# Kernel tuning notes

Measured on AMD Instinct MI355X. Metric: run time of the kernel, lower is better.

## Reference

```python
import jax, jax.numpy as jnp
import numpy as np

HIDDEN = 1024
STATE = 16
EXPAND = 2
INNER = HIDDEN * EXPAND
BATCH, SEQ = 4, 2048


def setup_inputs() -> dict:
    key = jax.random.key(0)
    ks = jax.random.split(key, 12)
    s = 0.02
    return {
        "x": jax.random.normal(ks[0], (BATCH, SEQ, HIDDEN), jnp.float32),
        "norm_scale": jnp.ones((HIDDEN,), jnp.float32),
        "norm_bias": jnp.zeros((HIDDEN,), jnp.float32),
        "W_in": jax.random.normal(ks[1], (HIDDEN, 2 * INNER), jnp.float32) * s,
        "conv_w": jax.random.normal(ks[2], (INNER, 3), jnp.float32) * 0.3,
        "conv_b": jnp.zeros((INNER,), jnp.float32),
        "W_dt": jax.random.normal(ks[3], (INNER, INNER), jnp.float32) * s,
        "b_dt": jnp.zeros((INNER,), jnp.float32),
        "A_log": jax.random.normal(ks[4], (INNER, STATE), jnp.float32),
        "D_param": jnp.ones((INNER,), jnp.float32),
        "W_B": jax.random.normal(ks[5], (INNER, STATE), jnp.float32) * s,
        "W_C": jax.random.normal(ks[6], (INNER, STATE), jnp.float32) * s,
        "W_out": jax.random.normal(ks[7], (INNER, HIDDEN), jnp.float32) * s,
    }


def reference(x, norm_scale, norm_bias, W_in, conv_w, conv_b, W_dt, b_dt,
              A_log, D_param, W_B, W_C, W_out):
    residual = x
    # LayerNorm (eps = 1e-5, matches nn.LayerNorm default)
    mu = jnp.mean(x, axis=-1, keepdims=True)
    var = jnp.mean(jnp.square(x - mu), axis=-1, keepdims=True)
    xn = (x - mu) * jax.lax.rsqrt(var + 1e-5) * norm_scale + norm_bias

    xz = xn @ W_in                         # [B, L, 2*inner]
    xb, z = jnp.split(xz, 2, axis=-1)      # each [B, L, inner]

    # depthwise conv1d, kernel 3, padding 1 (cross-correlation as in torch)
    xp = jnp.pad(xb, ((0, 0), (1, 1), (0, 0)))
    xb = (conv_w[:, 0] * xp[:, :-2] + conv_w[:, 1] * xp[:, 1:-1]
          + conv_w[:, 2] * xp[:, 2:] + conv_b)
    xb = jax.nn.silu(xb)

    dt = jax.nn.softplus(xb @ W_dt + b_dt)  # [B, L, inner]
    A = -jnp.exp(A_log)                     # [inner, N]
    Bi = xb @ W_B                           # [B, L, N]
    Ci = xb @ W_C                           # [B, L, N]

    def step(h, inp):
        x_t, dt_t, B_t, C_t = inp           # [B,D], [B,D], [B,N], [B,N]
        A_bar = jnp.exp(dt_t[:, :, None] * A)                 # [B, D, N]
        h = A_bar * h + (dt_t * x_t)[:, :, None] * B_t[:, None, :]
        y_t = jnp.einsum('bdn,bn->bd', h, C_t)
        return h, y_t

    h0 = jnp.zeros((x.shape[0], INNER, STATE), x.dtype)
    xs = (jnp.swapaxes(xb, 0, 1), jnp.swapaxes(dt, 0, 1),
          jnp.swapaxes(Bi, 0, 1), jnp.swapaxes(Ci, 0, 1))
    _, y = jax.lax.scan(step, h0, xs)       # y: [L, B, D]
    y = jnp.swapaxes(y, 0, 1)

    y = (y + D_param * xb) * jax.nn.silu(z)
    return residual + y @ W_out
```

## Files before the change

### kernel.cpp

```cpp
#include <hip/hip_runtime.h>
#include <hip/hip_bf16.h>
#include <cstdint>
#include <cstddef>

#define B_DIM 4
#define L_DIM 2048
#define H_DIM 1024
#define D_DIM 2048
#define N_STATE 16
#define TOKENS (B_DIM * L_DIM)
#define CH 16
#define LC (L_DIM / CH)
#define NEXT 2304
#define NLIM2 2080

typedef __bf16 bf16x8 __attribute__((ext_vector_type(8)));
typedef float f32x4 __attribute__((ext_vector_type(4)));

__device__ __forceinline__ float sigmoidf_(float x) { return 1.f / (1.f + __expf(-x)); }
__device__ __forceinline__ float softplusf_(float x) {
  return fmaxf(x, 0.f) + log1pf(__expf(-fabsf(x)));
}
__device__ __forceinline__ void gl_lds16(const void* g, void* l) {
  __builtin_amdgcn_global_load_lds(
      (const __attribute__((address_space(1))) unsigned int*)g,
      (__attribute__((address_space(3))) unsigned int*)l, 16, 0, 0);
}

__global__ __launch_bounds__(256) void ln_kernel(const float* __restrict__ x,
    const float* __restrict__ gamma, const float* __restrict__ beta,
    __hip_bfloat16* __restrict__ out) {
  int row = blockIdx.x;
  int t = threadIdx.x;
  const float* px = x + (size_t)row * H_DIM;
  float4 v = *(const float4*)(px + t * 4);
  float s  = v.x + v.y + v.z + v.w;
  float ss = v.x * v.x + v.y * v.y + v.z * v.z + v.w * v.w;
  for (int off = 32; off > 0; off >>= 1) {
    s  += __shfl_down(s, off);
    ss += __shfl_down(ss, off);
  }
  __shared__ float red[8];
  __shared__ float stats[2];
  int wave = t >> 6, lane = t & 63;
  if (lane == 0) { red[wave] = s; red[4 + wave] = ss; }
  __syncthreads();
  if (t == 0) {
    float S  = red[0] + red[1] + red[2] + red[3];
    float SS = red[4] + red[5] + red[6] + red[7];
    float mu = S / H_DIM;
    float var = SS / H_DIM - mu * mu;
    stats[0] = mu;
    stats[1] = rsqrtf(var + 1e-5f);
  }
  __syncthreads();
  float mu = stats[0], rstd = stats[1];
  float4 g  = *(const float4*)(gamma + t * 4);
  float4 bt = *(const float4*)(beta + t * 4);
  __hip_bfloat16* po = out + (size_t)row * H_DIM + t * 4;
  po[0] = __float2bfloat16((v.x - mu) * rstd * g.x + bt.x);
  po[1] = __float2bfloat16((v.y - mu) * rstd * g.y + bt.y);
  po[2] = __float2bfloat16((v.z - mu) * rstd * g.z + bt.z);
  po[3] = __float2bfloat16((v.w - mu) * rstd * g.w + bt.w);
}

__global__ void transpose_bf16(const float* __restrict__ in,
                               __hip_bfloat16* __restrict__ out, int R, int C) {
  __shared__ float tile[32][33];
  int c0 = blockIdx.x * 32, r0 = blockIdx.y * 32;
  int tx = threadIdx.x, ty = threadIdx.y;
  for (int i = 0; i < 32; i += 8)
    tile[ty + i][tx] = in[(size_t)(r0 + ty + i) * C + c0 + tx];
  __syncthreads();
  for (int i = 0; i < 32; i += 8)
    out[(size_t)(c0 + ty + i) * R + r0 + tx] = __float2bfloat16(tile[tx][ty + i]);
}

__global__ __launch_bounds__(256) void wbc_transpose(const float* __restrict__ WB,
    const float* __restrict__ WC, __hip_bfloat16* __restrict__ Wext) {
  int tid = blockIdx.x * 256 + threadIdx.x;
  int c = tid & 31;
  int k0 = (tid >> 5) * 16;
  const float* W = (c < 16) ? WB : WC;
  int cc = c & 15;
  __hip_bfloat16* o = Wext + (size_t)(2048 + c) * D_DIM + k0;
  for (int kk = 0; kk < 16; ++kk)
    o[kk] = __float2bfloat16(W[(size_t)(k0 + kk) * N_STATE + cc]);
}

template <int MODE>
__global__ __launch_bounds__(512, 2) void gemm256(
    const __hip_bfloat16* __restrict__ A, const __hip_bfloat16* __restrict__ Bt,
    void* __restrict__ C0, void* __restrict__ C1, int nsplit, int nlimit,
    int K, int lda, int ldb, int ldc, int ntn,
    const float* __restrict__ bias, const float* __restrict__ resid) {
  __shared__ __hip_bfloat16 lds[65536];
  const int t = threadIdx.x;
  const int nwg = gridDim.x;
  int bid = blockIdx.x;
  int wgid = (bid & 7) * (nwg >> 3) + (bid >> 3);
  const int m0 = (wgid / ntn) * 256;
  const int n0 = (wgid % ntn) * 256;

  const int wave = t >> 6, lane = t & 63;
  const int wm = wave >> 2, wn = wave & 3;
  const int l16 = lane & 15, quad = lane >> 4;
  const int bh = wn >> 1;

  const int srow = t >> 3, cslot = t & 7;
  const int cdata = cslot ^ (srow & 7);
  const __hip_bfloat16* Ast = A + (size_t)(m0 + srow) * lda + cdata * 8;
  const __hip_bfloat16* Bst = Bt + (size_t)(n0 + srow) * ldb + cdata * 8;
  const int stoff = srow * 64 + cslot * 8;

  const int ch0 = quad ^ (l16 & 7);
  const int ch1 = ch0 ^ 4;
  const int aoff0 = wm * 8192 + l16 * 64 + ch0 * 8;
  const int aoff1 = wm * 8192 + l16 * 64 + ch1 * 8;
  const int boff0 = 16384 + bh * 8192 + ((wn & 1) * 64 + l16) * 64 + ch0 * 8;
  const int boff1 = 16384 + bh * 8192 + ((wn & 1) * 64 + l16) * 64 + ch1 * 8;

  const int NT = K >> 6;

#define STAGE_HT(dstb, mat, h, ktX) do {                                        \
    const __hip_bfloat16* g_ = ((mat) ? Bst : Ast)                              \
        + (size_t)((h) * 128) * ((mat) ? ldb : lda) + (size_t)(ktX) * 64;       \
    __hip_bfloat16* l_ = &lds[(dstb) + (mat) * 16384 + (h) * 8192 + stoff];     \
    gl_lds16(g_, l_);                                                           \
    gl_lds16(g_ + (size_t)64 * ((mat) ? ldb : lda), l_ + 4096);                 \
  } while (0)

#define RD_A(aP, i0, db_) do {                                                  \
    aP[0][0] = *(const bf16x8*)&lds[(db_) + aoff0 + (i0) * 1024];               \
    aP[0][1] = *(const bf16x8*)&lds[(db_) + aoff1 + (i0) * 1024];               \
    aP[1][0] = *(const bf16x8*)&lds[(db_) + aoff0 + ((i0) + 1) * 1024];         \
    aP[1][1] = *(const bf16x8*)&lds[(db_) + aoff1 + ((i0) + 1) * 1024];         \
  } while (0)

#define RD_B(db_) do {                                                          \
    _Pragma("unroll") for (int j = 0; j < 4; ++j) {                             \
      bB0[j] = *(const bf16x8*)&lds[(db_) + boff0 + j * 1024];                  \
      bB1[j] = *(const bf16x8*)&lds[(db_) + boff1 + j * 1024];                  \
    }                                                                           \
  } while (0)

#define MFMA_PAIR(aP, i0) do {                                                  \
    _Pragma("unroll") for (int j = 0; j < 4; ++j) {                             \
      acc[i0][j] = __builtin_amdgcn_mfma_f32_16x16x32_bf16(                     \
          aP[0][0], bB0[j], acc[i0][j], 0, 0, 0);                               \
      acc[i0][j] = __builtin_amdgcn_mfma_f32_16x16x32_bf16(                     \
          aP[0][1], bB1[j], acc[i0][j], 0, 0, 0);                               \
      acc[(i0) + 1][j] = __builtin_amdgcn_mfma_f32_16x16x32_bf16(               \
          aP[1][0], bB0[j], acc[(i0) + 1][j], 0, 0, 0);                         \
      acc[(i0) + 1][j] = __builtin_amdgcn_mfma_f32_16x16x32_bf16(               \
          aP[1][1], bB1[j], acc[(i0) + 1][j], 0, 0, 0);                         \
    }                                                                           \
  } while (0)

#define PH_GATE() do {                                                          \
    __builtin_amdgcn_s_barrier();                                               \
    asm volatile("s_waitcnt lgkmcnt(0)" ::: "memory");                          \
    __builtin_amdgcn_sched_barrier(0);                                          \
    __builtin_amdgcn_s_setprio(1);                                              \
  } while (0)

#define PH_END() do {                                                           \
    __builtin_amdgcn_s_setprio(0);                                              \
    __builtin_amdgcn_sched_barrier(0);                                          \
    __builtin_amdgcn_s_barrier();                                               \
    asm volatile("" ::: "memory");                                              \
    __builtin_amdgcn_sched_barrier(0);                                          \
  } while (0)

  f32x4 acc[8][4] = {};
  bf16x8 bB0[4], bB1[4];
  bf16x8 a01[2][2], a23[2][2], a45[2][2], a67[2][2];

  STAGE_HT(0, 1, 0, 0);
  STAGE_HT(0, 1, 1, 0);
  STAGE_HT(0, 0, 0, 0);
  STAGE_HT(0, 0, 1, 0);
  STAGE_HT(32768, 1, 0, 1);
  STAGE_HT(32768, 1, 1, 1);
  STAGE_HT(32768, 0, 0, 1);
  asm volatile("s_waitcnt vmcnt(6)" ::: "memory");
  __builtin_amdgcn_s_barrier();
  asm volatile("" ::: "memory");

  for (int kt = 0; kt < NT; ++kt) {
    const int db32 = (kt & 1) << 15;
    const int dn32 = db32 ^ 32768;
    const bool p1 = (kt + 1 < NT);
    const bool p2 = (kt + 2 < NT);
    RD_B(db32);
    RD_A(a01, 0, db32);
    if (p1) STAGE_HT(dn32, 0, 1, kt + 1);
    PH_GATE();
    MFMA_PAIR(a01, 0);
    PH_END();
    RD_A(a23, 2, db32);
    RD_A(a45, 4, db32);
    if (p2) STAGE_HT(db32, 1, 0, kt + 2);
    PH_GATE();
    MFMA_PAIR(a23, 2);
    PH_END();
    RD_A(a67, 6, db32);
    if (p2) STAGE_HT(db32, 1, 1, kt + 2);
    PH_GATE();
    MFMA_PAIR(a45, 4);
    PH_END();
    if (p2) STAGE_HT(db32, 0, 0, kt + 2);
    __builtin_amdgcn_s_barrier();
    __builtin_amdgcn_sched_barrier(0);
    __builtin_amdgcn_s_setprio(1);
    MFMA_PAIR(a67, 6);
    __builtin_amdgcn_s_setprio(0);
    __builtin_amdgcn_sched_barrier(0);
    if (p2) {
      asm volatile("s_waitcnt vmcnt(6)" ::: "memory");
    } else {
      asm volatile("s_waitcnt vmcnt(0)" ::: "memory");
    }
    __builtin_amdgcn_s_barrier();
    asm volatile("" ::: "memory");
    __builtin_amdgcn_sched_barrier(0);
  }

  const int row_base = m0 + wm * 128;
  const int col_base = n0 + wn * 64;
#pragma unroll
  for (int i = 0; i < 8; ++i) {
    const int row0 = row_base + i * 16 + quad * 4;
#pragma unroll
    for (int j = 0; j < 4; ++j) {
      const int col = col_base + j * 16 + l16;
      f32x4 v = acc[i][j];
      if (MODE == 0) {
#pragma unroll
        for (int r = 0; r < 4; ++r) {
          size_t idx = (size_t)(row0 + r) * ldc + col;
          ((float*)C0)[idx] = v[r] + resid[idx];
        }
      } else if (MODE == 1) {
        bool mainc = (col < nsplit);
        __hip_bfloat16* cb = mainc ? (__hip_bfloat16*)C0 : (__hip_bfloat16*)C1;
        int ccol = mainc ? col : col - nsplit;
#pragma unroll
        for (int r = 0; r < 4; ++r)
          cb[(size_t)(row0 + r) * ldc + ccol] = __float2bfloat16(v[r]);
      } else {
        if (col < nsplit) {
          float bb = bias[col];
#pragma unroll
          for (int r = 0; r < 4; ++r)
            ((__hip_bfloat16*)C0)[(size_t)(row0 + r) * ldc + col] =
                __float2bfloat16(softplusf_(v[r] + bb));
        } else if (col < nlimit) {
#pragma unroll
          for (int r = 0; r < 4; ++r)
            ((float*)C1)[(size_t)(row0 + r) * 128 + (col - nsplit)] = v[r];
        }
      }
    }
  }
#undef STAGE_HT
#undef RD_A
#undef RD_B
#undef MFMA_PAIR
#undef PH_GATE
#undef PH_END
}

__global__ __launch_bounds__(256) void conv_silu_kernel(const __hip_bfloat16* __restrict__ xb,
    const float* __restrict__ cw, const float* __restrict__ cb,
    __hip_bfloat16* __restrict__ xbc) {
  size_t i2 = (size_t)blockIdx.x * 256 + threadIdx.x;
  int dp = (int)(i2 & (D_DIM / 2 - 1));
  size_t tok = i2 >> 10;
  int l = (int)(tok & (L_DIM - 1));
  int d = dp * 2;
  const __hip_bfloat162* base = (const __hip_bfloat162*)xb + i2;
  __hip_bfloat162 cc = base[0];
  float v0 = cw[d * 3 + 1] * __bfloat162float(cc.x) + cb[d];
  float v1 = cw[d * 3 + 4] * __bfloat162float(cc.y) + cb[d + 1];
  if (l > 0) {
    __hip_bfloat162 pm = base[-(D_DIM / 2)];
    v0 += cw[d * 3 + 0] * __bfloat162float(pm.x);
    v1 += cw[d * 3 + 3] * __bfloat162float(pm.y);
  }
  if (l < L_DIM - 1) {
    __hip_bfloat162 pp = base[D_DIM / 2];
    v0 += cw[d * 3 + 2] * __bfloat162float(pp.x);
    v1 += cw[d * 3 + 5] * __bfloat162float(pp.y);
  }
  v0 = v0 * sigmoidf_(v0);
  v1 = v1 * sigmoidf_(v1);
  __hip_bfloat162 o;
  o.x = __float2bfloat16(v0);
  o.y = __float2bfloat16(v1);
  ((__hip_bfloat162*)xbc)[i2] = o;
}

__global__ __launch_bounds__(256) void scan1_kernel(const __hip_bfloat16* __restrict__ dt,
    const __hip_bfloat16* __restrict__ xbc, const float* __restrict__ BiCi,
    const float* __restrict__ A_log, float* __restrict__ hfin,
    float* __restrict__ dtsum) {
  __shared__ float Bsh[LC * N_STATE];
  int t = threadIdx.x;
  int d = blockIdx.x * 256 + t;
  int c = blockIdx.y, b = blockIdx.z;
  size_t base = (size_t)b * L_DIM + (size_t)c * LC;
  for (int idx = t; idx < LC * 4; idx += 256) {
    int row = idx >> 2, q = idx & 3;
    ((float4*)Bsh)[row * 4 + q] = *(const float4*)&BiCi[(base + row) * 128 + q * 4];
  }
  float Aneg[N_STATE];
  {
    const float4* Ap = (const float4*)(A_log + (size_t)d * N_STATE);
#pragma unroll
    for (int q = 0; q < 4; ++q) {
      float4 av = Ap[q];
      Aneg[4 * q + 0] = -__expf(av.x);
      Aneg[4 * q + 1] = -__expf(av.y);
      Aneg[4 * q + 2] = -__expf(av.z);
      Aneg[4 * q + 3] = -__expf(av.w);
    }
  }
  __syncthreads();
  const __hip_bfloat16* dtp = dt + base * D_DIM + d;
  const __hip_bfloat16* xp = xbc + base * D_DIM + d;
  float h[N_STATE];
#pragma unroll
  for (int n = 0; n < N_STATE; ++n) h[n] = 0.f;
  float ds = 0.f;
  float dtv = __bfloat162float(dtp[0]), xv = __bfloat162float(xp[0]);
  for (int i = 0; i < LC; ++i) {
    int ip = (i < LC - 1) ? i + 1 : i;
    float dt2 = __bfloat162float(dtp[(size_t)ip * D_DIM]);
    float x2  = __bfloat162float(xp[(size_t)ip * D_DIM]);
    float dtx = dtv * xv;
    ds += dtv;
    const float4* Brow = (const float4*)&Bsh[i * N_STATE];
#pragma unroll
    for (int q = 0; q < 4; ++q) {
      float4 bv = Brow[q];
      h[4*q+0] = __expf(dtv * Aneg[4*q+0]) * h[4*q+0] + dtx * bv.x;
      h[4*q+1] = __expf(dtv * Aneg[4*q+1]) * h[4*q+1] + dtx * bv.y;
      h[4*q+2] = __expf(dtv * Aneg[4*q+2]) * h[4*q+2] + dtx * bv.z;
      h[4*q+3] = __expf(dtv * Aneg[4*q+3]) * h[4*q+3] + dtx * bv.w;
    }
    dtv = dt2; xv = x2;
  }
  float* ho = hfin + (((size_t)b * CH + c) * D_DIM + d) * N_STATE;
#pragma unroll
  for (int q = 0; q < 4; ++q) {
    float4 v; v.x = h[4*q]; v.y = h[4*q+1]; v.z = h[4*q+2]; v.w = h[4*q+3];
    ((float4*)ho)[q] = v;
  }
  dtsum[((size_t)b * CH + c) * D_DIM + d] = ds;
}

__global__ __launch_bounds__(256) void scan2_kernel(const float* __restrict__ hfin,
    const float* __restrict__ dtsum, const float* __restrict__ A_log,
    float* __restrict__ hstart) {
  int tid = blockIdx.x * 256 + threadIdx.x;
  int n = tid & 15;
  int d = (tid >> 4) & (D_DIM - 1);
  int b = tid >> 15;
  float Aneg = -__expf(A_log[d * N_STATE + n]);
  float run = 0.f;
  for (int c = 0; c < CH; ++c) {
    size_t o = (((size_t)b * CH + c) * D_DIM + d) * N_STATE + n;
    hstart[o] = run;
    run = __expf(Aneg * dtsum[((size_t)b * CH + c) * D_DIM + d]) * run + hfin[o];
  }
}

__global__ __launch_bounds__(256) void scan3_kernel(const __hip_bfloat16* __restrict__ dt,
    const __hip_bfloat16* __restrict__ xbc, const float* __restrict__ BiCi,
    const float* __restrict__ A_log,
    const float* __restrict__ hstart, const __hip_bfloat16* __restrict__ z,
    const float* __restrict__ Dp, __hip_bfloat16* __restrict__ yo) {
  __shared__ float Bsh[LC * N_STATE];
  __shared__ float Csh[LC * N_STATE];
  int t = threadIdx.x;
  int d = blockIdx.x * 256 + t;
  int c = blockIdx.y, b = blockIdx.z;
  size_t base = (size_t)b * L_DIM + (size_t)c * LC;
  for (int idx = t; idx < LC * 4; idx += 256) {
    int row = idx >> 2, q = idx & 3;
    ((float4*)Bsh)[row * 4 + q] = *(const float4*)&BiCi[(base + row) * 128 + q * 4];
    ((float4*)Csh)[row * 4 + q] = *(const float4*)&BiCi[(base + row) * 128 + 16 + q * 4];
  }
  float Aneg[N_STATE];
  {
    const float4* Ap = (const float4*)(A_log + (size_t)d * N_STATE);
#pragma unroll
    for (int q = 0; q < 4; ++q) {
      float4 av = Ap[q];
      Aneg[4 * q + 0] = -__expf(av.x);
      Aneg[4 * q + 1] = -__expf(av.y);
      Aneg[4 * q + 2] = -__expf(av.z);
      Aneg[4 * q + 3] = -__expf(av.w);
    }
  }
  float h[N_STATE];
  {
    const float4* hs = (const float4*)(hstart + (((size_t)b * CH + c) * D_DIM + d) * N_STATE);
#pragma unroll
    for (int q = 0; q < 4; ++q) {
      float4 v = hs[q];
      h[4*q] = v.x; h[4*q+1] = v.y; h[4*q+2] = v.z; h[4*q+3] = v.w;
    }
  }
  float Dv = Dp[d];
  __syncthreads();
  const __hip_bfloat16* dtp = dt + base * D_DIM + d;
  const __hip_bfloat16* xp = xbc + base * D_DIM + d;
  const __hip_bfloat16* zp = z + base * D_DIM + d;
  __hip_bfloat16* yp = yo + base * D_DIM + d;
  float dtv = __bfloat162float(dtp[0]), xv = __bfloat162float(xp[0]);
  float zv = __bfloat162float(zp[0]);
  for (int i = 0; i < LC; ++i) {
    int ip = (i < LC - 1) ? i + 1 : i;
    float dt2 = __bfloat162float(dtp[(size_t)ip * D_DIM]);
    float x2  = __bfloat162float(xp[(size_t)ip * D_DIM]);
    float z2  = __bfloat162float(zp[(size_t)ip * D_DIM]);
    float dtx = dtv * xv;
    const float4* Brow = (const float4*)&Bsh[i * N_STATE];
    const float4* Crow = (const float4*)&Csh[i * N_STATE];
    float yv = 0.f;
#pragma unroll
    for (int q = 0; q < 4; ++q) {
      float4 bv = Brow[q];
      float4 cv = Crow[q];
      h[4*q+0] = __expf(dtv * Aneg[4*q+0]) * h[4*q+0] + dtx * bv.x;
      h[4*q+1] = __expf(dtv * Aneg[4*q+1]) * h[4*q+1] + dtx * bv.y;
      h[4*q+2] = __expf(dtv * Aneg[4*q+2]) * h[4*q+2] + dtx * bv.z;
      h[4*q+3] = __expf(dtv * Aneg[4*q+3]) * h[4*q+3] + dtx * bv.w;
      yv += h[4*q+0] * cv.x + h[4*q+1] * cv.y + h[4*q+2] * cv.z + h[4*q+3] * cv.w;
    }
    float g = zv * sigmoidf_(zv);
    yp[(size_t)i * D_DIM] = __float2bfloat16((yv + Dv * xv) * g);
    dtv = dt2; xv = x2; zv = z2;
  }
}

extern "C" void kernel_launch(void* const* d_in, const int* in_sizes, int n_in,
                              void* d_out, int out_size, void* d_ws, size_t ws_size,
                              hipStream_t stream) {
  const float* x          = (const float*)d_in[0];
  const float* norm_scale = (const float*)d_in[1];
  const float* norm_bias  = (const float*)d_in[2];
  const float* W_in       = (const float*)d_in[3];
  const float* conv_w     = (const float*)d_in[4];
  const float* conv_b     = (const float*)d_in[5];
  const float* W_dt       = (const float*)d_in[6];
  const float* b_dt       = (const float*)d_in[7];
  const float* A_log      = (const float*)d_in[8];
  const float* D_param    = (const float*)d_in[9];
  const float* W_B        = (const float*)d_in[10];
  const float* W_C        = (const float*)d_in[11];
  const float* W_out      = (const float*)d_in[12];
  float* out = (float*)d_out;

  const size_t MB = 1024 * 1024;
  const size_t NEEDED = 193 * MB;
  if (ws_size < NEEDED) return;

  char* ws = (char*)d_ws;
  __hip_bfloat16* xn     = (__hip_bfloat16*)(ws);
  __hip_bfloat16* W_outT = (__hip_bfloat16*)(ws);
  float*          hfin   = (float*)(ws + 4 * MB);
  float*          dtsum  = (float*)(ws + 12 * MB);
  __hip_bfloat16* xb     = (__hip_bfloat16*)(ws + 16 * MB);
  __hip_bfloat16* ybf    = (__hip_bfloat16*)(ws + 16 * MB);
  __hip_bfloat16* z      = (__hip_bfloat16*)(ws + 48 * MB);
  __hip_bfloat16* xbc    = (__hip_bfloat16*)(ws + 80 * MB);
  __hip_bfloat16* dtY    = (__hip_bfloat16*)(ws + 112 * MB);
  float*          BiCi   = (float*)(ws + 144 * MB);
  __hip_bfloat16* W_ext  = (__hip_bfloat16*)(ws + 148 * MB);
  __hip_bfloat16* W_inT  = (__hip_bfloat16*)(ws + 177 * MB);
  float*          hstart = (float*)(ws + 177 * MB);

  dim3 tb(32, 8);
  transpose_bf16<<<dim3(4096 / 32, 1024 / 32), tb, 0, stream>>>(W_in, W_inT, 1024, 4096);
  transpose_bf16<<<dim3(2048 / 32, 2048 / 32), tb, 0, stream>>>(W_dt, W_ext, 2048, 2048);
  wbc_transpose<<<16, 256, 0, stream>>>(W_B, W_C, W_ext);
  ln_kernel<<<TOKENS, 256, 0, stream>>>(x, norm_scale, norm_bias, xn);
  gemm256<1><<<(TOKENS / 256) * (4096 / 256), 512, 0, stream>>>(
      xn, W_inT, xb, z, D_DIM, 1 << 30, H_DIM, H_DIM, H_DIM, D_DIM, 4096 / 256,
      nullptr, nullptr);
  transpose_bf16<<<dim3(1024 / 32, 2048 / 32), tb, 0, stream>>>(W_out, W_outT, 2048, 1024);
  conv_silu_kernel<<<(TOKENS * D_DIM / 2) / 256, 256, 0, stream>>>(xb, conv_w, conv_b, xbc);
  gemm256<2><<<(TOKENS / 256) * (NEXT / 256), 512, 0, stream>>>(
      xbc, W_ext, dtY, BiCi, D_DIM, NLIM2, D_DIM, D_DIM, D_DIM, D_DIM, NEXT / 256,
      b_dt, nullptr);
  scan1_kernel<<<dim3(D_DIM / 256, CH, B_DIM), 256, 0, stream>>>(
      dtY, xbc, BiCi, A_log, hfin, dtsum);
  scan2_kernel<<<(B_DIM * D_DIM * N_STATE) / 256, 256, 0, stream>>>(
      hfin, dtsum, A_log, hstart);
  scan3_kernel<<<dim3(D_DIM / 256, CH, B_DIM), 256, 0, stream>>>(
      dtY, xbc, BiCi, A_log, hstart, z, D_param, ybf);
  gemm256<0><<<(TOKENS / 256) * (1024 / 256), 512, 0, stream>>>(
      ybf, W_outT, out, nullptr, 1 << 30, 1 << 30, D_DIM, D_DIM, D_DIM, H_DIM,
      1024 / 256, nullptr, x);
}
```

Measured before the change: 671.3 us.

## Use a 128x128 GEMM for the output projection and relax scheduling fences

Adds a simpler 128x128x64 bf16 MFMA GEMM kernel with XOR-swizzled LDS and grouped block ordering, and routes the final W_out projection (with residual add) through it instead of the 256x256 pipelined kernel. The goal is better occupancy and more blocks for the N=1024 output GEMM, where 256-wide tiles give few workgroups. The large GEMM's phase gates lose their explicit lgkmcnt waits and sched_barriers, leaving plain barriers and priority changes. Without those fences the compiler is free to reorder the LDS reads, and correctness then depends on the waits it inserts itself. The new kernel is single-buffered with two syncthreads per K step, so it has less load/compute overlap.

```diff
diff --git a/kernel.cpp b/kernel.cpp
--- a/kernel.cpp
+++ b/kernel.cpp
@@ -157,21 +157,6 @@
     }                                                                           \
   } while (0)
 
-#define PH_GATE() do {                                                          \
-    __builtin_amdgcn_s_barrier();                                               \
-    asm volatile("s_waitcnt lgkmcnt(0)" ::: "memory");                          \
-    __builtin_amdgcn_sched_barrier(0);                                          \
-    __builtin_amdgcn_s_setprio(1);                                              \
-  } while (0)
-
-#define PH_END() do {                                                           \
-    __builtin_amdgcn_s_setprio(0);                                              \
-    __builtin_amdgcn_sched_barrier(0);                                          \
-    __builtin_amdgcn_s_barrier();                                               \
-    asm volatile("" ::: "memory");                                              \
-    __builtin_amdgcn_sched_barrier(0);                                          \
-  } while (0)
-
   f32x4 acc[8][4] = {};
   bf16x8 bB0[4], bB1[4];
   bf16x8 a01[2][2], a23[2][2], a45[2][2], a67[2][2];
@@ -185,7 +170,6 @@
   STAGE_HT(32768, 0, 0, 1);
   asm volatile("s_waitcnt vmcnt(6)" ::: "memory");
   __builtin_amdgcn_s_barrier();
-  asm volatile("" ::: "memory");
 
   for (int kt = 0; kt < NT; ++kt) {
     const int db32 = (kt & 1) << 15;
@@ -195,35 +179,37 @@
     RD_B(db32);
     RD_A(a01, 0, db32);
     if (p1) STAGE_HT(dn32, 0, 1, kt + 1);
-    PH_GATE();
+    __builtin_amdgcn_s_barrier();
+    __builtin_amdgcn_s_setprio(1);
     MFMA_PAIR(a01, 0);
-    PH_END();
+    __builtin_amdgcn_s_setprio(0);
+    __builtin_amdgcn_s_barrier();
     RD_A(a23, 2, db32);
     RD_A(a45, 4, db32);
     if (p2) STAGE_HT(db32, 1, 0, kt + 2);
-    PH_GATE();
+    __builtin_amdgcn_s_barrier();
+    __builtin_amdgcn_s_setprio(1);
     MFMA_PAIR(a23, 2);
-    PH_END();
+    __builtin_amdgcn_s_setprio(0);
+    __builtin_amdgcn_s_barrier();
     RD_A(a67, 6, db32);
     if (p2) STAGE_HT(db32, 1, 1, kt + 2);
-    PH_GATE();
+    __builtin_amdgcn_s_barrier();
+    __builtin_amdgcn_s_setprio(1);
     MFMA_PAIR(a45, 4);
-    PH_END();
+    __builtin_amdgcn_s_setprio(0);
+    __builtin_amdgcn_s_barrier();
     if (p2) STAGE_HT(db32, 0, 0, kt + 2);
     __builtin_amdgcn_s_barrier();
-    __builtin_amdgcn_sched_barrier(0);
     __builtin_amdgcn_s_setprio(1);
     MFMA_PAIR(a67, 6);
     __builtin_amdgcn_s_setprio(0);
-    __builtin_amdgcn_sched_barrier(0);
     if (p2) {
       asm volatile("s_waitcnt vmcnt(6)" ::: "memory");
     } else {
       asm volatile("s_waitcnt vmcnt(0)" ::: "memory");
     }
     __builtin_amdgcn_s_barrier();
-    asm volatile("" ::: "memory");
-    __builtin_amdgcn_sched_barrier(0);
   }
 
   const int row_base = m0 + wm * 128;
@@ -267,8 +253,109 @@
 #undef RD_A
 #undef RD_B
 #undef MFMA_PAIR
-#undef PH_GATE
-#undef PH_END
+}
+
+#define BM 128
+#define BN 128
+#define BK 64
+
+template <int MODE>
+__global__ __launch_bounds__(256) void gemm_bf16(
+    const __hip_bfloat16* __restrict__ A, const __hip_bfloat16* __restrict__ Bt,
+    void* __restrict__ C0, void* __restrict__ C1, int nsplit,
+    int K, int lda, int ldb, int ldc, int gx,
+    const float* __restrict__ bias, const float* __restrict__ resid) {
+  __shared__ __hip_bfloat16 As[BM * BK];
+  __shared__ __hip_bfloat16 Bs[BN * BK];
+  int t = threadIdx.x;
+  int bid = blockIdx.x;
+  int nsup = gx << 3;
+  int super = bid / nsup;
+  int rem = bid - super * nsup;
+  int m0 = (super * 8 + (rem & 7)) * BM;
+  int n0 = (rem >> 3) * BN;
+
+  int wave = t >> 6, lane = t & 63;
+  int quad = lane >> 4, l16 = lane & 15;
+  int wm = (wave >> 1) * 64, wn = (wave & 1) * 64;
+
+  f32x4 acc[4][4] = {};
+
+  int srow  = t >> 3;
+  int cslot = t & 7;
+  int cdata = cslot ^ (srow & 7);
+  const __hip_bfloat16* Ag[4];
+  const __hip_bfloat16* Bg[4];
+  __hip_bfloat16* Asl[4];
+  __hip_bfloat16* Bsl[4];
+#pragma unroll
+  for (int j = 0; j < 4; ++j) {
+    Ag[j]  = A  + (size_t)(m0 + j * 32 + srow) * lda + cdata * 8;
+    Bg[j]  = Bt + (size_t)(n0 + j * 32 + srow) * ldb + cdata * 8;
+    Asl[j] = &As[(j * 32 + srow) * BK + cslot * 8];
+    Bsl[j] = &Bs[(j * 32 + srow) * BK + cslot * 8];
+  }
+
+  for (int k0 = 0; k0 < K; k0 += BK) {
+    __syncthreads();
+#pragma unroll
+    for (int j = 0; j < 4; ++j) {
+      gl_lds16(Ag[j] + k0, Asl[j]);
+      gl_lds16(Bg[j] + k0, Bsl[j]);
+    }
+    __syncthreads();
+#pragma unroll
+    for (int s = 0; s < 2; ++s) {
+      int cs = ((s * 4 + quad) ^ (l16 & 7)) * 8;
+      bf16x8 af[4], bf_[4];
+#pragma unroll
+      for (int i = 0; i < 4; ++i) {
+        af[i]  = *(const bf16x8*)&As[(wm + i * 16 + l16) * BK + cs];
+        bf_[i] = *(const bf16x8*)&Bs[(wn + i * 16 + l16) * BK + cs];
+      }
+#pragma unroll
+      for (int i = 0; i < 4; ++i)
+#pragma unroll
+        for (int j = 0; j < 4; ++j)
+          acc[i][j] = __builtin_amdgcn_mfma_f32_16x16x32_bf16(af[i], bf_[j], acc[i][j], 0, 0, 0);
+    }
+  }
+
+#pragma unroll
+  for (int i = 0; i < 4; ++i) {
+    int row0 = m0 + wm + i * 16 + quad * 4;
+#pragma unroll
+    for (int j = 0; j < 4; ++j) {
+      int col = n0 + wn + j * 16 + l16;
+      f32x4 v = acc[i][j];
+      if (MODE == 0) {
+#pragma unroll
+        for (int r = 0; r < 4; ++r) {
+          size_t idx = (size_t)(row0 + r) * ldc + col;
+          ((float*)C0)[idx] = v[r] + resid[idx];
+        }
+      } else if (MODE == 1) {
+        bool mainc = (col < nsplit);
+        __hip_bfloat16* cb = mainc ? (__hip_bfloat16*)C0 : (__hip_bfloat16*)C1;
+        int ccol = mainc ? col : col - nsplit;
+#pragma unroll
+        for (int r = 0; r < 4; ++r)
+          cb[(size_t)(row0 + r) * ldc + ccol] = __float2bfloat16(v[r]);
+      } else {
+        if (col < nsplit) {
+          float bb = bias[col];
+#pragma unroll
+          for (int r = 0; r < 4; ++r)
+            ((__hip_bfloat16*)C0)[(size_t)(row0 + r) * ldc + col] =
+                __float2bfloat16(softplusf_(v[r] + bb));
+        } else {
+#pragma unroll
+          for (int r = 0; r < 4; ++r)
+            ((float*)C1)[(size_t)(row0 + r) * 128 + (col - nsplit)] = v[r];
+        }
+      }
+    }
+  }
 }
 
 __global__ __launch_bounds__(256) void conv_silu_kernel(const __hip_bfloat16* __restrict__ xb,
@@ -502,7 +589,7 @@
       hfin, dtsum, A_log, hstart);
   scan3_kernel<<<dim3(D_DIM / 256, CH, B_DIM), 256, 0, stream>>>(
       dtY, xbc, BiCi, A_log, hstart, z, D_param, ybf);
-  gemm256<0><<<(TOKENS / 256) * (1024 / 256), 512, 0, stream>>>(
-      ybf, W_outT, out, nullptr, 1 << 30, 1 << 30, D_DIM, D_DIM, D_DIM, H_DIM,
-      1024 / 256, nullptr, x);
-}
+  gemm_bf16<0><<<(H_DIM / BN) * (TOKENS / BM), 256, 0, stream>>>(
+      ybf, W_outT, out, nullptr, 1 << 30, D_DIM, D_DIM, D_DIM, H_DIM, H_DIM / BN,
+      nullptr, x);
+}
```

New measurement: 646.9 us. 3.6% less time.
